# Optimization experiments

Measured on AMD Instinct MI355X. Metric: run time of the kernel, lower is better.

The kernel has to match this reference:

```python
import jax, jax.numpy as jnp
import numpy as np

N = 100000   # nodes
E = 1600000  # edges
FEAT = 128
HID = 128
TGT = 64
L = 3
G = 512      # graphs in batch


def setup_inputs() -> dict:
    key = jax.random.key(0)
    ks = jax.random.split(key, 16)
    s = 0.05
    return {
        "x": jax.random.normal(ks[0], (N, FEAT), jnp.float32),
        "edge_index": jax.random.randint(ks[1], (2, E), 0, N, dtype=jnp.int32),
        "batch": jnp.sort(jax.random.randint(ks[2], (N,), 0, G, dtype=jnp.int32)),
        "conv_w1": jax.random.normal(ks[3], (L, FEAT, HID), jnp.float32) * s,
        "conv_b1": jax.random.normal(ks[4], (L, HID), jnp.float32) * s,
        "conv_w2": jax.random.normal(ks[5], (L, HID, HID), jnp.float32) * s,
        "conv_b2": jax.random.normal(ks[6], (L, HID), jnp.float32) * s,
        "eps": jnp.zeros((L,), jnp.float32),
        "gn_scale": jnp.ones((L, HID), jnp.float32),
        "gn_weight": jnp.ones((L, HID), jnp.float32),
        "gn_bias": jnp.zeros((L, HID), jnp.float32),
        "proj_w1": jax.random.normal(ks[7], (L, HID, HID), jnp.float32) * s,
        "proj_b1": jax.random.normal(ks[8], (L, HID), jnp.float32) * s,
        "proj_w2": jax.random.normal(ks[9], (L, HID, TGT), jnp.float32) * s,
        "proj_b2": jax.random.normal(ks[10], (L, TGT), jnp.float32) * s,
    }


def _graph_norm(h, batch, counts, scale, weight, bias):
    # per-graph mean -> scatter back to nodes
    mean = jax.ops.segment_sum(h, batch, num_segments=G) / counts
    sub = h - mean[batch] * scale
    var = jax.ops.segment_sum(sub * sub, batch, num_segments=G) / counts
    std = jnp.sqrt(var + 1e-8)
    return weight * sub / std[batch] + bias


def reference(x, edge_index, batch, conv_w1, conv_b1, conv_w2, conv_b2, eps,
              gn_scale, gn_weight, gn_bias, proj_w1, proj_b1, proj_w2, proj_b2):
    src, dst = edge_index[0], edge_index[1]
    counts = jnp.maximum(
        jax.ops.segment_sum(jnp.ones((N, 1), x.dtype), batch, num_segments=G), 1.0)
    h = x
    z_cat = []
    for l in range(L):
        # GINConv: aggr_j->i then 2-layer MLP
        aggr = jax.ops.segment_sum(h[src], dst, num_segments=N)
        h = (1.0 + eps[l]) * h + aggr
        h = jax.nn.relu(h @ conv_w1[l] + conv_b1[l]) @ conv_w2[l] + conv_b2[l]
        # GraphNorm
        h = _graph_norm(h, batch, counts, gn_scale[l], gn_weight[l], gn_bias[l])
        h = jax.nn.relu(h)
        # projection MLP + global add pool
        z = jax.nn.relu(h @ proj_w1[l] + proj_b1[l]) @ proj_w2[l] + proj_b2[l]
        z_cat.append(jax.ops.segment_sum(z, batch, num_segments=G))
    return jnp.concatenate(z_cat, axis=-1)  # [G, L*TGT]
```

## Files before the change

kernel.cpp:

```cpp
#include <hip/hip_runtime.h>

#define NN 100000
#define EE 1600000
#define HIDD 128
#define TGTT 64
#define GGG 512
#define NBK 98
#define CAPB 17408
#define ABLK 200
#define LSTR 136

typedef unsigned short ushort_t;
typedef __attribute__((ext_vector_type(8))) short short8;
typedef __attribute__((ext_vector_type(4))) float f32x4;
typedef __attribute__((ext_vector_type(4))) unsigned short us4;

__device__ __forceinline__ float b2f(ushort_t u) {
    union { unsigned int i; float f; } v; v.i = ((unsigned int)u) << 16; return v.f;
}
__device__ __forceinline__ ushort_t f2b(float f) {
    union { float f; unsigned int i; } v; v.f = f;
    unsigned int r = (v.i + 0x7fffu + ((v.i >> 16) & 1u)) >> 16;
    return (ushort_t)r;
}

__global__ void k_goff(const int* __restrict__ batch, int* __restrict__ goff) {
    int t = blockIdx.x * blockDim.x + threadIdx.x;
    if (t > GGG) return;
    int lo = 0, hi = NN;
    while (lo < hi) { int mid = (lo + hi) >> 1; if (batch[mid] < t) lo = mid + 1; else hi = mid; }
    goff[t] = lo;
}

__global__ __launch_bounds__(256) void k_cvt(const float* __restrict__ x, ushort_t* __restrict__ Xb) {
    long i = (long)blockIdx.x * 256 + threadIdx.x;
    if (i >= (long)NN * 32) return;
    float4 v = ((const float4*)x)[i];
    us4 o; o.x = f2b(v.x); o.y = f2b(v.y); o.z = f2b(v.z); o.w = f2b(v.w);
    ((us4*)Xb)[i] = o;
}

__global__ __launch_bounds__(256) void k_prep(const float* __restrict__ cw1, const float* __restrict__ cw2,
                                              const float* __restrict__ pw1, ushort_t* __restrict__ Wt) {
    __shared__ ushort_t sW[128 * 129];
    int mat = blockIdx.x;
    int l = mat / 3, j = mat % 3;
    const float* src = (j == 0 ? cw1 : j == 1 ? cw2 : pw1) + (size_t)l * HIDD * HIDD;
    ushort_t* dst = Wt + (size_t)mat * HIDD * HIDD;
    for (int i = threadIdx.x; i < HIDD * HIDD; i += 256) {
        int k = i >> 7, n = i & 127;
        sW[n * 129 + k] = f2b(src[i]);
    }
    __syncthreads();
    for (int i = threadIdx.x; i < HIDD * HIDD; i += 256) {
        dst[i] = sW[(i >> 7) * 129 + (i & 127)];
    }
}

__global__ __launch_bounds__(256) void k_binA(const int* __restrict__ ei,
                                              int* __restrict__ gcnt,
                                              unsigned int* __restrict__ bbuf) {
    __shared__ int cnt[NBK], base[NBK], cur[NBK];
    int t = threadIdx.x;
    if (t < NBK) cnt[t] = 0;
    __syncthreads();
    int e0 = blockIdx.x * 8000;
    int e1 = min(e0 + 8000, EE);
    for (int e = e0 + t; e < e1; e += 256)
        atomicAdd(&cnt[ei[EE + e] >> 10], 1);
    __syncthreads();
    if (t < NBK) { base[t] = atomicAdd(&gcnt[t], cnt[t]); cur[t] = 0; }
    __syncthreads();
    for (int e = e0 + t; e < e1; e += 256) {
        int s = ei[e], d = ei[EE + e];
        int b = d >> 10;
        int off = base[b] + atomicAdd(&cur[b], 1);
        if (off < CAPB)
            bbuf[(long)b * CAPB + off] = (unsigned int)s | (((unsigned int)d & 1023u) << 17);
    }
}

__global__ void k_bbase(const int* __restrict__ gcnt, int* __restrict__ gbase,
                        int* __restrict__ rowptr) {
    __shared__ int sd[128];
    int t = threadIdx.x;
    int v = (t < NBK) ? gcnt[t] : 0;
    sd[t] = v;
    __syncthreads();
    for (int off = 1; off < 128; off <<= 1) {
        int u = (t >= off) ? sd[t - off] : 0;
        __syncthreads();
        sd[t] += u;
        __syncthreads();
    }
    if (t < NBK) gbase[t] = sd[t] - v;
    if (t == 0) rowptr[NN] = EE;
}

__global__ __launch_bounds__(256) void k_csr(const int* __restrict__ gcnt,
                                             const int* __restrict__ gbase,
                                             const unsigned int* __restrict__ bbuf,
                                             int* __restrict__ rowptr, int* __restrict__ csr) {
    __shared__ int ldeg[1024], lcur[1024], tsum[256];
    int b = blockIdx.x, t = threadIdx.x;
    int cnt = min(gcnt[b], CAPB);
    int base = gbase[b];
    const unsigned int* bb = bbuf + (long)b * CAPB;
#pragma unroll
    for (int i = 0; i < 4; i++) ldeg[t + 256 * i] = 0;
    __syncthreads();
    for (int i = t; i < cnt; i += 256) atomicAdd(&ldeg[bb[i] >> 17], 1);
    __syncthreads();
    int d0 = ldeg[4 * t], d1 = ldeg[4 * t + 1], d2 = ldeg[4 * t + 2], d3 = ldeg[4 * t + 3];
    int tot = d0 + d1 + d2 + d3;
    tsum[t] = tot;
    __syncthreads();
    for (int off = 1; off < 256; off <<= 1) {
        int u = (t >= off) ? tsum[t - off] : 0;
        __syncthreads();
        tsum[t] += u;
        __syncthreads();
    }
    int texcl = tsum[t] - tot;
    int p0 = base + texcl, p1 = p0 + d0, p2 = p1 + d1, p3 = p2 + d2;
    lcur[4 * t] = p0; lcur[4 * t + 1] = p1; lcur[4 * t + 2] = p2; lcur[4 * t + 3] = p3;
    int gnode = b * 1024 + 4 * t;
    if (gnode < NN)     rowptr[gnode]     = p0;
    if (gnode + 1 < NN) rowptr[gnode + 1] = p1;
    if (gnode + 2 < NN) rowptr[gnode + 2] = p2;
    if (gnode + 3 < NN) rowptr[gnode + 3] = p3;
    __syncthreads();
    for (int i = t; i < cnt; i += 256) {
        unsigned int en = bb[i];
        int pos = atomicAdd(&lcur[en >> 17], 1);
        csr[pos] = (int)(en & 0x1FFFFu);
    }
}

__global__ __launch_bounds__(256) void k_gmlp(const ushort_t* __restrict__ hin,
                                              const int* __restrict__ rowptr,
                                              const int* __restrict__ csr,
                                              const float* __restrict__ eps, int l,
                                              const ushort_t* __restrict__ Wt1, const float* __restrict__ B1,
                                              const ushort_t* __restrict__ Wt2, const float* __restrict__ B2,
                                              ushort_t* __restrict__ Y) {
    __shared__ ushort_t sX[128 * LSTR];
    int tid = threadIdx.x;
    long base = (long)blockIdx.x * 128;
    int lane = tid & 15, ng = tid >> 4;
    int off = lane << 3;
    float e1 = 1.0f + eps[l];

#pragma unroll 1
    for (int it = 0; it < 8; it++) {
        int row = it * 16 + ng;
        long node = base + row;
        short8 o = (short8)0;
        if (node < NN) {
            short8 h = *(const short8*)(hin + (node << 7) + off);
            float acc[8];
#pragma unroll
            for (int t = 0; t < 8; t++) acc[t] = e1 * b2f((ushort_t)h[t]);
            int jb = rowptr[node], je = rowptr[node + 1];
            int j = jb;
            for (; j + 8 <= je; j += 8) {
                int s0 = csr[j], s1 = csr[j + 1], s2 = csr[j + 2], s3 = csr[j + 3];
                int s4 = csr[j + 4], s5 = csr[j + 5], s6 = csr[j + 6], s7 = csr[j + 7];
                short8 v0 = *(const short8*)(hin + ((long)s0 << 7) + off);
                short8 v1 = *(const short8*)(hin + ((long)s1 << 7) + off);
                short8 v2 = *(const short8*)(hin + ((long)s2 << 7) + off);
                short8 v3 = *(const short8*)(hin + ((long)s3 << 7) + off);
                short8 v4 = *(const short8*)(hin + ((long)s4 << 7) + off);
                short8 v5 = *(const short8*)(hin + ((long)s5 << 7) + off);
                short8 v6 = *(const short8*)(hin + ((long)s6 << 7) + off);
                short8 v7 = *(const short8*)(hin + ((long)s7 << 7) + off);
#pragma unroll
                for (int t = 0; t < 8; t++)
                    acc[t] += ((b2f((ushort_t)v0[t]) + b2f((ushort_t)v1[t])) +
                               (b2f((ushort_t)v2[t]) + b2f((ushort_t)v3[t]))) +
                              ((b2f((ushort_t)v4[t]) + b2f((ushort_t)v5[t])) +
                               (b2f((ushort_t)v6[t]) + b2f((ushort_t)v7[t])));
            }
            for (; j + 4 <= je; j += 4) {
                int s0 = csr[j], s1 = csr[j + 1], s2 = csr[j + 2], s3 = csr[j + 3];
                short8 v0 = *(const short8*)(hin + ((long)s0 << 7) + off);
                short8 v1 = *(const short8*)(hin + ((long)s1 << 7) + off);
                short8 v2 = *(const short8*)(hin + ((long)s2 << 7) + off);
                short8 v3 = *(const short8*)(hin + ((long)s3 << 7) + off);
#pragma unroll
                for (int t = 0; t < 8; t++)
                    acc[t] += (b2f((ushort_t)v0[t]) + b2f((ushort_t)v1[t])) +
                              (b2f((ushort_t)v2[t]) + b2f((ushort_t)v3[t]));
            }
            for (; j < je; j++) {
                int s = csr[j];
                short8 v = *(const short8*)(hin + ((long)s << 7) + off);
#pragma unroll
                for (int t = 0; t < 8; t++) acc[t] += b2f((ushort_t)v[t]);
            }
#pragma unroll
            for (int t = 0; t < 8; t++) o[t] = (short)f2b(acc[t]);
        }
        *(short8*)(sX + row * LSTR + off) = o;
    }
    __syncthreads();

    int w = tid >> 6, l64 = tid & 63, q = l64 >> 4, l16 = l64 & 15;
    int r0 = w * 16, r1 = 64 + w * 16;
    short8 a0[4], a1[4];
#pragma unroll
    for (int c = 0; c < 4; c++) {
        a0[c] = *(const short8*)(sX + (r0 + l16) * LSTR + q * 8 + c * 32);
        a1[c] = *(const short8*)(sX + (r1 + l16) * LSTR + q * 8 + c * 32);
    }
    f32x4 acc0[8], acc1[8];
#pragma unroll
    for (int nt = 0; nt < 8; nt++) {
        int col = nt * 16 + l16;
        float bias = B1[col];
        f32x4 c0 = {bias, bias, bias, bias};
        f32x4 c1 = c0;
        const ushort_t* bB = Wt1 + col * HIDD + q * 8;
#pragma unroll
        for (int c = 0; c < 4; c++) {
            short8 b = *(const short8*)(bB + c * 32);
            c0 = __builtin_amdgcn_mfma_f32_16x16x32_bf16(a0[c], b, c0, 0, 0, 0);
            c1 = __builtin_amdgcn_mfma_f32_16x16x32_bf16(a1[c], b, c1, 0, 0, 0);
        }
        acc0[nt] = c0; acc1[nt] = c1;
    }
    __syncthreads();
#pragma unroll
    for (int nt = 0; nt < 8; nt++) {
        int col = nt * 16 + l16;
#pragma unroll
        for (int r = 0; r < 4; r++) {
            sX[(r0 + q * 4 + r) * LSTR + col] = f2b(fmaxf(acc0[nt][r], 0.f));
            sX[(r1 + q * 4 + r) * LSTR + col] = f2b(fmaxf(acc1[nt][r], 0.f));
        }
    }
    __syncthreads();
#pragma unroll
    for (int c = 0; c < 4; c++) {
        a0[c] = *(const short8*)(sX + (r0 + l16) * LSTR + q * 8 + c * 32);
        a1[c] = *(const short8*)(sX + (r1 + l16) * LSTR + q * 8 + c * 32);
    }
#pragma unroll
    for (int nt = 0; nt < 8; nt++) {
        int col = nt * 16 + l16;
        float bias = B2[col];
        f32x4 c0 = {bias, bias, bias, bias};
        f32x4 c1 = c0;
        const ushort_t* bB = Wt2 + col * HIDD + q * 8;
#pragma unroll
        for (int c = 0; c < 4; c++) {
            short8 b = *(const short8*)(bB + c * 32);
            c0 = __builtin_amdgcn_mfma_f32_16x16x32_bf16(a0[c], b, c0, 0, 0, 0);
            c1 = __builtin_amdgcn_mfma_f32_16x16x32_bf16(a1[c], b, c1, 0, 0, 0);
        }
#pragma unroll
        for (int r = 0; r < 4; r++) {
            long row0 = base + r0 + q * 4 + r;
            long row1 = base + r1 + q * 4 + r;
            if (row0 < NN) Y[(row0 << 7) + col] = f2b(c0[r]);
            if (row1 < NN) Y[(row1 << 7) + col] = f2b(c1[r]);
        }
    }
}

__global__ __launch_bounds__(512) void k_gstat(const ushort_t* __restrict__ Hraw,
                                               const int* __restrict__ goff,
                                               const float* __restrict__ scale,
                                               const float* __restrict__ weight,
                                               float* __restrict__ msb, float* __restrict__ invb,
                                               float* __restrict__ pooled) {
    int g = blockIdx.x;
    int s = goff[g], e = goff[g + 1];
    float cnt = (float)max(e - s, 1);
    int fp = threadIdx.x & 63;
    int r = threadIdx.x >> 6;
    int f0 = fp * 2;
    float s0 = 0.f, s1 = 0.f, q0 = 0.f, q1 = 0.f;
    for (int i = s + r; i < e; i += 8) {
        unsigned int v = *(const unsigned int*)(Hraw + ((long)i << 7) + f0);
        float a = b2f((ushort_t)(v & 0xffffu));
        float b = b2f((ushort_t)(v >> 16));
        s0 += a; q0 += a * a; s1 += b; q1 += b * b;
    }
    __shared__ float red[4][8][64];
    red[0][r][fp] = s0; red[1][r][fp] = q0; red[2][r][fp] = s1; red[3][r][fp] = q1;
    __syncthreads();
    if (r == 0) {
#pragma unroll
        for (int k = 1; k < 8; k++) {
            s0 += red[0][k][fp]; q0 += red[1][k][fp];
            s1 += red[2][k][fp]; q1 += red[3][k][fp];
        }
        float mean0 = s0 / cnt, mean1 = s1 / cnt;
        float ms0 = mean0 * scale[f0], ms1 = mean1 * scale[f0 + 1];
        float var0 = q0 / cnt - 2.f * ms0 * mean0 + ms0 * ms0;
        float var1 = q1 / cnt - 2.f * ms1 * mean1 + ms1 * ms1;
        msb[g * HIDD + f0] = ms0;
        msb[g * HIDD + f0 + 1] = ms1;
        invb[g * HIDD + f0] = weight[f0] / sqrtf(var0 + 1e-8f);
        invb[g * HIDD + f0 + 1] = weight[f0 + 1] / sqrtf(var1 + 1e-8f);
        pooled[g * HIDD + f0] = 0.f;
        pooled[g * HIDD + f0 + 1] = 0.f;
    }
}

__global__ __launch_bounds__(256) void k_projpool(const ushort_t* __restrict__ Hraw,
                                                  const int* __restrict__ batch,
                                                  const float* __restrict__ msb, const float* __restrict__ invb,
                                                  const float* __restrict__ gnb,
                                                  const ushort_t* __restrict__ Wt, const float* __restrict__ B,
                                                  ushort_t* __restrict__ Hn, float* __restrict__ pooled) {
    __shared__ ushort_t sX[128 * LSTR];
    __shared__ int sgid[128];
    int tid = threadIdx.x;
    long base = (long)blockIdx.x * 128;
#pragma unroll
    for (int c = 0; c < 8; c++) {
        int idx = c * 256 + tid;
        int row = idx >> 4, cw = idx & 15;
        long grow = base + row;
        short8 v = (short8)0;
        if (grow < NN) {
            short8 raw = *(const short8*)(Hraw + (grow << 7) + (cw << 3));
            int g = batch[grow];
            if (cw == 0) sgid[row] = g;
            const float* msp = msb + g * HIDD + (cw << 3);
            const float* ivp = invb + g * HIDD + (cw << 3);
            const float* gbp = gnb + (cw << 3);
            float4 m0 = *(const float4*)msp, m1 = *(const float4*)(msp + 4);
            float4 i0 = *(const float4*)ivp, i1 = *(const float4*)(ivp + 4);
            float4 g0 = *(const float4*)gbp, g1 = *(const float4*)(gbp + 4);
            float mv[8] = {m0.x, m0.y, m0.z, m0.w, m1.x, m1.y, m1.z, m1.w};
            float iv[8] = {i0.x, i0.y, i0.z, i0.w, i1.x, i1.y, i1.z, i1.w};
            float gv[8] = {g0.x, g0.y, g0.z, g0.w, g1.x, g1.y, g1.z, g1.w};
#pragma unroll
            for (int t = 0; t < 8; t++) {
                float val = (b2f((ushort_t)raw[t]) - mv[t]) * iv[t] + gv[t];
                v[t] = (short)f2b(val > 0.f ? val : 0.f);
            }
            *(short8*)(Hn + (grow << 7) + (cw << 3)) = v;
        } else if (cw == 0) {
            sgid[row] = -1;
        }
        *(short8*)(sX + row * LSTR + (cw << 3)) = v;
    }
    __syncthreads();

    int w = tid >> 6, l64 = tid & 63, q = l64 >> 4, l16 = l64 & 15;
    int r0 = w * 16, r1 = 64 + w * 16;
    short8 a0[4], a1[4];
#pragma unroll
    for (int c = 0; c < 4; c++) {
        a0[c] = *(const short8*)(sX + (r0 + l16) * LSTR + q * 8 + c * 32);
        a1[c] = *(const short8*)(sX + (r1 + l16) * LSTR + q * 8 + c * 32);
    }
    f32x4 acc0[8], acc1[8];
#pragma unroll
    for (int nt = 0; nt < 8; nt++) {
        int col = nt * 16 + l16;
        float bias = B[col];
        f32x4 c0 = {bias, bias, bias, bias};
        f32x4 c1 = c0;
        const ushort_t* bB = Wt + col * HIDD + q * 8;
#pragma unroll
        for (int c = 0; c < 4; c++) {
            short8 b = *(const short8*)(bB + c * 32);
            c0 = __builtin_amdgcn_mfma_f32_16x16x32_bf16(a0[c], b, c0, 0, 0, 0);
            c1 = __builtin_amdgcn_mfma_f32_16x16x32_bf16(a1[c], b, c1, 0, 0, 0);
        }
        acc0[nt] = c0; acc1[nt] = c1;
    }
    __syncthreads();
#pragma unroll
    for (int nt = 0; nt < 8; nt++) {
        int col = nt * 16 + l16;
#pragma unroll
        for (int r = 0; r < 4; r++) {
            sX[(r0 + q * 4 + r) * LSTR + col] = f2b(fmaxf(acc0[nt][r], 0.f));
            sX[(r1 + q * 4 + r) * LSTR + col] = f2b(fmaxf(acc1[nt][r], 0.f));
        }
    }
    __syncthreads();

    int f = tid & 127, half = tid >> 7;
    int rbeg = half * 64, rend = rbeg + 64;
    float sum = 0.f;
    int curg = -1;
    for (int row = rbeg; row < rend; row++) {
        int g = sgid[row];
        if (g != curg) {
            if (curg >= 0) atomicAdd(&pooled[(long)curg * HIDD + f], sum);
            sum = 0.f; curg = g;
        }
        if (g >= 0) sum += b2f(sX[row * LSTR + f]);
    }
    if (curg >= 0) atomicAdd(&pooled[(long)curg * HIDD + f], sum);
}

__global__ __launch_bounds__(64) void k_out(const float* __restrict__ pooled, const int* __restrict__ goff,
                                            const float* __restrict__ W, const float* __restrict__ B,
                                            float* __restrict__ out, int l) {
    int g = blockIdx.x;
    int t = threadIdx.x;
    __shared__ float p[128];
    p[t] = pooled[g * HIDD + t];
    p[t + 64] = pooled[g * HIDD + 64 + t];
    __syncthreads();
    float cnt = (float)(goff[g + 1] - goff[g]);
    float acc = cnt * B[t];
    for (int k = 0; k < HIDD; k++) acc += p[k] * W[k * TGTT + t];
    out[(long)g * (3 * TGTT) + l * TGTT + t] = acc;
}

extern "C" void kernel_launch(void* const* d_in, const int* in_sizes, int n_in,
                              void* d_out, int out_size, void* d_ws, size_t ws_size,
                              hipStream_t stream) {
    const float* x    = (const float*)d_in[0];
    const int*   ei   = (const int*)d_in[1];
    const int*   batch= (const int*)d_in[2];
    const float* cw1  = (const float*)d_in[3];
    const float* cb1  = (const float*)d_in[4];
    const float* cw2  = (const float*)d_in[5];
    const float* cb2  = (const float*)d_in[6];
    const float* eps  = (const float*)d_in[7];
    const float* gsc  = (const float*)d_in[8];
    const float* gw   = (const float*)d_in[9];
    const float* gb   = (const float*)d_in[10];
    const float* pw1  = (const float*)d_in[11];
    const float* pb1  = (const float*)d_in[12];
    const float* pw2  = (const float*)d_in[13];
    const float* pb2  = (const float*)d_in[14];
    float* out = (float*)d_out;

    ushort_t* Xb   = (ushort_t*)d_ws;
    ushort_t* Hn   = Xb;
    ushort_t* Hraw = Xb + (size_t)NN * HIDD;
    ushort_t* Wt   = Hraw + (size_t)NN * HIDD;
    float* msb     = (float*)(Wt + (size_t)9 * HIDD * HIDD);
    float* invb    = msb + (size_t)GGG * HIDD;
    float* pooled  = invb + (size_t)GGG * HIDD;
    int* goff   = (int*)(pooled + (size_t)GGG * HIDD);
    int* rowptr = goff + (GGG + 1);
    int* gcnt   = rowptr + (NN + 1);
    int* gbase  = gcnt + NBK;
    int* csr    = gbase + NBK;
    unsigned int* bbuf = (unsigned int*)(csr + EE);

    k_goff<<<3, 256, 0, stream>>>(batch, goff);
    k_cvt<<<(int)(((long)NN * 32 + 255) / 256), 256, 0, stream>>>(x, Xb);
    k_prep<<<9, 256, 0, stream>>>(cw1, cw2, pw1, Wt);

    hipMemsetAsync(gcnt, 0, NBK * sizeof(int), stream);
    k_binA<<<ABLK, 256, 0, stream>>>(ei, gcnt, bbuf);
    k_bbase<<<1, 128, 0, stream>>>(gcnt, gbase, rowptr);
    k_csr<<<NBK, 256, 0, stream>>>(gcnt, gbase, bbuf, rowptr, csr);

    for (int l = 0; l < 3; l++) {
        const ushort_t* hin = (l == 0) ? Xb : Hn;
        ushort_t* Wt1 = Wt + (size_t)(l * 3 + 0) * HIDD * HIDD;
        ushort_t* Wt2 = Wt + (size_t)(l * 3 + 1) * HIDD * HIDD;
        ushort_t* Wtp = Wt + (size_t)(l * 3 + 2) * HIDD * HIDD;
        k_gmlp<<<(NN + 127) / 128, 256, 0, stream>>>(hin, rowptr, csr, eps, l,
                                                     Wt1, cb1 + l * HIDD, Wt2, cb2 + l * HIDD, Hraw);
        k_gstat<<<GGG, 512, 0, stream>>>(Hraw, goff, gsc + l * HIDD, gw + l * HIDD, msb, invb, pooled);
        k_projpool<<<(NN + 127) / 128, 256, 0, stream>>>(Hraw, batch, msb, invb, gb + l * HIDD,
                                                         Wtp, pb1 + l * HIDD, Hn, pooled);
        k_out<<<GGG, 64, 0, stream>>>(pooled, goff, pw2 + (size_t)l * HIDD * TGTT, pb2 + l * TGTT, out, l);
    }
}
```

Before: 642.2 us.

## Merge prologue kernels and fold output projection into next layer's GIN kernel

The conversion, weight-transpose, graph-offset and edge-binning kernels become one launch that dispatches on block index, and the bucket prefix scan moves into k_csr, where each block redoes it. The per-layer output projection for layer l-1 runs as extra blocks of layer l's k_gmlp launch, leaving one final k_out. The last layer also skips writing the normalized node features it never reads. The aim is fewer kernel launches and their gaps. The cost is a redundant serial scan per CSR block and a larger, branchier fused kernel.

```diff
diff --git a/kernel.cpp b/kernel.cpp
--- a/kernel.cpp
+++ b/kernel.cpp
@@ -9,6 +9,9 @@
 #define CAPB 17408
 #define ABLK 200
 #define LSTR 136
+#define CVTB 3125
+#define GBLK 782
+#define OUTB 128
 
 typedef unsigned short ushort_t;
 typedef __attribute__((ext_vector_type(8))) short short8;
@@ -24,87 +27,83 @@
     return (ushort_t)r;
 }
 
-__global__ void k_goff(const int* __restrict__ batch, int* __restrict__ goff) {
-    int t = blockIdx.x * blockDim.x + threadIdx.x;
-    if (t > GGG) return;
-    int lo = 0, hi = NN;
-    while (lo < hi) { int mid = (lo + hi) >> 1; if (batch[mid] < t) lo = mid + 1; else hi = mid; }
-    goff[t] = lo;
-}
-
-__global__ __launch_bounds__(256) void k_cvt(const float* __restrict__ x, ushort_t* __restrict__ Xb) {
-    long i = (long)blockIdx.x * 256 + threadIdx.x;
-    if (i >= (long)NN * 32) return;
-    float4 v = ((const float4*)x)[i];
-    us4 o; o.x = f2b(v.x); o.y = f2b(v.y); o.z = f2b(v.z); o.w = f2b(v.w);
-    ((us4*)Xb)[i] = o;
-}
-
-__global__ __launch_bounds__(256) void k_prep(const float* __restrict__ cw1, const float* __restrict__ cw2,
-                                              const float* __restrict__ pw1, ushort_t* __restrict__ Wt) {
+__global__ __launch_bounds__(256) void k_pro(const float* __restrict__ x, ushort_t* __restrict__ Xb,
+                                             const float* __restrict__ cw1, const float* __restrict__ cw2,
+                                             const float* __restrict__ pw1, ushort_t* __restrict__ Wt,
+                                             const int* __restrict__ batch, int* __restrict__ goff,
+                                             const int* __restrict__ ei, int* __restrict__ gcnt,
+                                             unsigned int* __restrict__ bbuf) {
     __shared__ ushort_t sW[128 * 129];
-    int mat = blockIdx.x;
-    int l = mat / 3, j = mat % 3;
-    const float* src = (j == 0 ? cw1 : j == 1 ? cw2 : pw1) + (size_t)l * HIDD * HIDD;
-    ushort_t* dst = Wt + (size_t)mat * HIDD * HIDD;
-    for (int i = threadIdx.x; i < HIDD * HIDD; i += 256) {
-        int k = i >> 7, n = i & 127;
-        sW[n * 129 + k] = f2b(src[i]);
-    }
-    __syncthreads();
-    for (int i = threadIdx.x; i < HIDD * HIDD; i += 256) {
-        dst[i] = sW[(i >> 7) * 129 + (i & 127)];
-    }
-}
-
-__global__ __launch_bounds__(256) void k_binA(const int* __restrict__ ei,
-                                              int* __restrict__ gcnt,
-                                              unsigned int* __restrict__ bbuf) {
     __shared__ int cnt[NBK], base[NBK], cur[NBK];
-    int t = threadIdx.x;
-    if (t < NBK) cnt[t] = 0;
-    __syncthreads();
-    int e0 = blockIdx.x * 8000;
-    int e1 = min(e0 + 8000, EE);
-    for (int e = e0 + t; e < e1; e += 256)
-        atomicAdd(&cnt[ei[EE + e] >> 10], 1);
-    __syncthreads();
-    if (t < NBK) { base[t] = atomicAdd(&gcnt[t], cnt[t]); cur[t] = 0; }
-    __syncthreads();
-    for (int e = e0 + t; e < e1; e += 256) {
-        int s = ei[e], d = ei[EE + e];
-        int b = d >> 10;
-        int off = base[b] + atomicAdd(&cur[b], 1);
-        if (off < CAPB)
-            bbuf[(long)b * CAPB + off] = (unsigned int)s | (((unsigned int)d & 1023u) << 17);
-    }
-}
-
-__global__ void k_bbase(const int* __restrict__ gcnt, int* __restrict__ gbase,
-                        int* __restrict__ rowptr) {
-    __shared__ int sd[128];
-    int t = threadIdx.x;
-    int v = (t < NBK) ? gcnt[t] : 0;
-    sd[t] = v;
-    __syncthreads();
-    for (int off = 1; off < 128; off <<= 1) {
-        int u = (t >= off) ? sd[t - off] : 0;
-        __syncthreads();
-        sd[t] += u;
-        __syncthreads();
-    }
-    if (t < NBK) gbase[t] = sd[t] - v;
-    if (t == 0) rowptr[NN] = EE;
+    int b = blockIdx.x, t = threadIdx.x;
+
+    if (b < CVTB) {
+        long i0 = (long)b * 1024 + t;
+#pragma unroll
+        for (int c = 0; c < 4; c++) {
+            long i = i0 + c * 256;
+            float4 v = ((const float4*)x)[i];
+            us4 o; o.x = f2b(v.x); o.y = f2b(v.y); o.z = f2b(v.z); o.w = f2b(v.w);
+            ((us4*)Xb)[i] = o;
+        }
+        return;
+    }
+    b -= CVTB;
+    if (b < 9) {
+        int l = b / 3, j = b % 3;
+        const float* src = (j == 0 ? cw1 : j == 1 ? cw2 : pw1) + (size_t)l * HIDD * HIDD;
+        ushort_t* dst = Wt + (size_t)b * HIDD * HIDD;
+        for (int i = t; i < HIDD * HIDD; i += 256) {
+            int k = i >> 7, n = i & 127;
+            sW[n * 129 + k] = f2b(src[i]);
+        }
+        __syncthreads();
+        for (int i = t; i < HIDD * HIDD; i += 256) {
+            dst[i] = sW[(i >> 7) * 129 + (i & 127)];
+        }
+        return;
+    }
+    b -= 9;
+    if (b < 3) {
+        int g = b * 256 + t;
+        if (g > GGG) return;
+        int lo = 0, hi = NN;
+        while (lo < hi) { int mid = (lo + hi) >> 1; if (batch[mid] < g) lo = mid + 1; else hi = mid; }
+        goff[g] = lo;
+        return;
+    }
+    b -= 3;
+    {
+        if (t < NBK) cnt[t] = 0;
+        __syncthreads();
+        int e0 = b * 8000;
+        int e1 = min(e0 + 8000, EE);
+        for (int e = e0 + t; e < e1; e += 256)
+            atomicAdd(&cnt[ei[EE + e] >> 10], 1);
+        __syncthreads();
+        if (t < NBK) { base[t] = atomicAdd(&gcnt[t], cnt[t]); cur[t] = 0; }
+        __syncthreads();
+        for (int e = e0 + t; e < e1; e += 256) {
+            int s = ei[e], d = ei[EE + e];
+            int bk = d >> 10;
+            int off = base[bk] + atomicAdd(&cur[bk], 1);
+            if (off < CAPB)
+                bbuf[(long)bk * CAPB + off] = (unsigned int)s | (((unsigned int)d & 1023u) << 17);
+        }
+    }
 }
 
 __global__ __launch_bounds__(256) void k_csr(const int* __restrict__ gcnt,
-                                             const int* __restrict__ gbase,
                                              const unsigned int* __restrict__ bbuf,
                                              int* __restrict__ rowptr, int* __restrict__ csr) {
-    __shared__ int ldeg[1024], lcur[1024], tsum[256];
+    __shared__ int ldeg[1024], lcur[1024], tsum[256], sb[NBK];
     int b = blockIdx.x, t = threadIdx.x;
+    if (t < NBK) sb[t] = gcnt[t];
+    __syncthreads();
+    if (t == 0) { int a = 0; for (int i = 0; i < NBK; i++) { int v = sb[i]; sb[i] = a; a += v; } }
+    __syncthreads();
     int cnt = min(gcnt[b], CAPB);
-    int base = gbase[b];
+    int base = sb[b];
     const unsigned int* bb = bbuf + (long)b * CAPB;
 #pragma unroll
     for (int i = 0; i < 4; i++) ldeg[t + 256 * i] = 0;
@@ -129,6 +128,7 @@
     if (gnode + 1 < NN) rowptr[gnode + 1] = p1;
     if (gnode + 2 < NN) rowptr[gnode + 2] = p2;
     if (gnode + 3 < NN) rowptr[gnode + 3] = p3;
+    if (b == NBK - 1 && t == 0) rowptr[NN] = EE;
     __syncthreads();
     for (int i = t; i < cnt; i += 256) {
         unsigned int en = bb[i];
@@ -143,9 +143,27 @@
                                               const float* __restrict__ eps, int l,
                                               const ushort_t* __restrict__ Wt1, const float* __restrict__ B1,
                                               const ushort_t* __restrict__ Wt2, const float* __restrict__ B2,
-                                              ushort_t* __restrict__ Y) {
+                                              ushort_t* __restrict__ Y,
+                                              const float* __restrict__ pooledP, const int* __restrict__ goff,
+                                              const float* __restrict__ WoP, const float* __restrict__ BoP,
+                                              float* __restrict__ outP, int lprev) {
     __shared__ ushort_t sX[128 * LSTR];
     int tid = threadIdx.x;
+
+    if (blockIdx.x >= GBLK) {
+        if (lprev < 0) return;
+        int ob = blockIdx.x - GBLK;
+        int sub = tid >> 6, tt = tid & 63;
+        int g = ob * 4 + sub;
+        if (g >= GGG) return;
+        float cntg = (float)(goff[g + 1] - goff[g]);
+        float acc = cntg * BoP[tt];
+        const float* p = pooledP + (long)g * HIDD;
+        for (int k = 0; k < HIDD; k++) acc += p[k] * WoP[k * TGTT + tt];
+        outP[(long)g * (3 * TGTT) + lprev * TGTT + tt] = acc;
+        return;
+    }
+
     long base = (long)blockIdx.x * 128;
     int lane = tid & 15, ng = tid >> 4;
     int off = lane << 3;
@@ -314,7 +332,8 @@
                                                   const float* __restrict__ msb, const float* __restrict__ invb,
                                                   const float* __restrict__ gnb,
                                                   const ushort_t* __restrict__ Wt, const float* __restrict__ B,
-                                                  ushort_t* __restrict__ Hn, float* __restrict__ pooled) {
+                                                  ushort_t* __restrict__ Hn, float* __restrict__ pooled,
+                                                  int store_hn) {
     __shared__ ushort_t sX[128 * LSTR];
     __shared__ int sgid[128];
     int tid = threadIdx.x;
@@ -343,7 +362,7 @@
                 float val = (b2f((ushort_t)raw[t]) - mv[t]) * iv[t] + gv[t];
                 v[t] = (short)f2b(val > 0.f ? val : 0.f);
             }
-            *(short8*)(Hn + (grow << 7) + (cw << 3)) = v;
+            if (store_hn) *(short8*)(Hn + (grow << 7) + (cw << 3)) = v;
         } else if (cw == 0) {
             sgid[row] = -1;
         }
@@ -402,19 +421,17 @@
     if (curg >= 0) atomicAdd(&pooled[(long)curg * HIDD + f], sum);
 }
 
-__global__ __launch_bounds__(64) void k_out(const float* __restrict__ pooled, const int* __restrict__ goff,
-                                            const float* __restrict__ W, const float* __restrict__ B,
-                                            float* __restrict__ out, int l) {
-    int g = blockIdx.x;
-    int t = threadIdx.x;
-    __shared__ float p[128];
-    p[t] = pooled[g * HIDD + t];
-    p[t + 64] = pooled[g * HIDD + 64 + t];
-    __syncthreads();
+__global__ __launch_bounds__(256) void k_out(const float* __restrict__ pooled, const int* __restrict__ goff,
+                                             const float* __restrict__ W, const float* __restrict__ B,
+                                             float* __restrict__ out, int l) {
+    int sub = threadIdx.x >> 6, tt = threadIdx.x & 63;
+    int g = blockIdx.x * 4 + sub;
+    if (g >= GGG) return;
     float cnt = (float)(goff[g + 1] - goff[g]);
-    float acc = cnt * B[t];
-    for (int k = 0; k < HIDD; k++) acc += p[k] * W[k * TGTT + t];
-    out[(long)g * (3 * TGTT) + l * TGTT + t] = acc;
+    float acc = cnt * B[tt];
+    const float* p = pooled + (long)g * HIDD;
+    for (int k = 0; k < HIDD; k++) acc += p[k] * W[k * TGTT + tt];
+    out[(long)g * (3 * TGTT) + l * TGTT + tt] = acc;
 }
 
 extern "C" void kernel_launch(void* const* d_in, const int* in_sizes, int n_in,
@@ -447,29 +464,27 @@
     int* goff   = (int*)(pooled + (size_t)GGG * HIDD);
     int* rowptr = goff + (GGG + 1);
     int* gcnt   = rowptr + (NN + 1);
-    int* gbase  = gcnt + NBK;
-    int* csr    = gbase + NBK;
+    int* csr    = gcnt + NBK;
     unsigned int* bbuf = (unsigned int*)(csr + EE);
 
-    k_goff<<<3, 256, 0, stream>>>(batch, goff);
-    k_cvt<<<(int)(((long)NN * 32 + 255) / 256), 256, 0, stream>>>(x, Xb);
-    k_prep<<<9, 256, 0, stream>>>(cw1, cw2, pw1, Wt);
-
     hipMemsetAsync(gcnt, 0, NBK * sizeof(int), stream);
-    k_binA<<<ABLK, 256, 0, stream>>>(ei, gcnt, bbuf);
-    k_bbase<<<1, 128, 0, stream>>>(gcnt, gbase, rowptr);
-    k_csr<<<NBK, 256, 0, stream>>>(gcnt, gbase, bbuf, rowptr, csr);
+    k_pro<<<CVTB + 9 + 3 + ABLK, 256, 0, stream>>>(x, Xb, cw1, cw2, pw1, Wt, batch, goff, ei, gcnt, bbuf);
+    k_csr<<<NBK, 256, 0, stream>>>(gcnt, bbuf, rowptr, csr);
 
     for (int l = 0; l < 3; l++) {
         const ushort_t* hin = (l == 0) ? Xb : Hn;
         ushort_t* Wt1 = Wt + (size_t)(l * 3 + 0) * HIDD * HIDD;
         ushort_t* Wt2 = Wt + (size_t)(l * 3 + 1) * HIDD * HIDD;
         ushort_t* Wtp = Wt + (size_t)(l * 3 + 2) * HIDD * HIDD;
-        k_gmlp<<<(NN + 127) / 128, 256, 0, stream>>>(hin, rowptr, csr, eps, l,
-                                                     Wt1, cb1 + l * HIDD, Wt2, cb2 + l * HIDD, Hraw);
+        int grid = GBLK + (l > 0 ? OUTB : 0);
+        k_gmlp<<<grid, 256, 0, stream>>>(hin, rowptr, csr, eps, l,
+                                         Wt1, cb1 + l * HIDD, Wt2, cb2 + l * HIDD, Hraw,
+                                         pooled, goff,
+                                         pw2 + (size_t)(l - 1) * HIDD * TGTT, pb2 + (l - 1) * TGTT,
+                                         out, l - 1);
         k_gstat<<<GGG, 512, 0, stream>>>(Hraw, goff, gsc + l * HIDD, gw + l * HIDD, msb, invb, pooled);
-        k_projpool<<<(NN + 127) / 128, 256, 0, stream>>>(Hraw, batch, msb, invb, gb + l * HIDD,
-                                                         Wtp, pb1 + l * HIDD, Hn, pooled);
-        k_out<<<GGG, 64, 0, stream>>>(pooled, goff, pw2 + (size_t)l * HIDD * TGTT, pb2 + l * TGTT, out, l);
-    }
-}
+        k_projpool<<<GBLK, 256, 0, stream>>>(Hraw, batch, msb, invb, gb + l * HIDD,
+                                             Wtp, pb1 + l * HIDD, Hn, pooled, (l < 2) ? 1 : 0);
+    }
+    k_out<<<OUTB, 256, 0, stream>>>(pooled, goff, pw2 + (size_t)2 * HIDD * TGTT, pb2 + 2 * TGTT, out, 2);
+}
```

Measured after the change: 614.5 us. -4.3%, faster.
